# Kernel tuning notes

Measured on AMD Instinct MI355X. Metric: run time of the kernel, lower is better.

The kernel has to match this reference:

```python
import jax, jax.numpy as jnp
import numpy as np

B, C, D = 16384, 1000, 512
CLAMP_MIN = 1e-12
CLAMP_MAX = 1e12


def setup_inputs() -> dict:
    key = jax.random.key(0)
    k1, k2, k3 = jax.random.split(key, 3)
    x = jax.random.normal(k1, (B, D), dtype=jnp.float32)
    labels = jax.random.randint(k2, (B,), 0, C, dtype=jnp.int64)
    # centers param: n_classes != feat_dim -> normal init (as in _init_centers)
    centers = jax.random.normal(k3, (C, D), dtype=jnp.float32)
    return {"x": x, "labels": labels, "centers": centers}


def reference(x, labels, centers):
    batch_size = x.shape[0]
    n_classes = centers.shape[0]
    x_sq = jnp.sum(x * x, axis=1, keepdims=True)            # [B, 1]
    c_sq = jnp.sum(centers * centers, axis=1)[None, :]      # [1, C]
    distmat = x_sq + c_sq - 2.0 * (x @ centers.T)           # [B, C]
    # one-hot mask on true label
    mask = (labels[:, None] == jnp.arange(n_classes)[None, :]).astype(distmat.dtype)
    # NOTE: torch code clamps AFTER masking, so masked-out zeros become 1e-12
    # and each contributes 1e-12 to the sum -- reproduce that faithfully.
    dist = jnp.clip(distmat * mask, CLAMP_MIN, CLAMP_MAX)
    loss = jnp.sum(dist) / batch_size
    return loss
```

## Files before the change

### kernel.cpp

```cpp
#include <hip/hip_runtime.h>


#define B_ROWS    16384
#define C_CLASSES 1000
#define D_DIM     512
#define S1_BLOCKS 1024

__global__ __launch_bounds__(256) void center_loss_stage1(
    const float* __restrict__ x,
    const int*   __restrict__ labels,
    const float* __restrict__ centers,
    float*       __restrict__ partials)
{
    const int tid   = threadIdx.x;
    const int wave  = tid >> 6;
    const int lane  = tid & 63;
    const int gwave = blockIdx.x * 4 + wave;
    const int nwaves = gridDim.x * 4;

    float waveAcc = 0.0f;

    for (int row = gwave; row < B_ROWS; row += nwaves) {
        const int lab = labels[row];
        const float4* __restrict__ xr =
            (const float4*)(x + (size_t)row * D_DIM);
        const float4* __restrict__ cr =
            (const float4*)(centers + (size_t)lab * D_DIM);

        float4 xa = xr[lane];
        float4 xb = xr[lane + 64];
        float4 ca = cr[lane];
        float4 cb = cr[lane + 64];

        float d0 = xa.x - ca.x, d1 = xa.y - ca.y;
        float d2 = xa.z - ca.z, d3 = xa.w - ca.w;
        float e0 = xb.x - cb.x, e1 = xb.y - cb.y;
        float e2 = xb.z - cb.z, e3 = xb.w - cb.w;

        float s = d0*d0 + d1*d1 + d2*d2 + d3*d3
                + e0*e0 + e1*e1 + e2*e2 + e3*e3;

        #pragma unroll
        for (int off = 32; off > 0; off >>= 1)
            s += __shfl_down(s, off, 64);

        if (lane == 0) {
            s = fminf(fmaxf(s, 1e-12f), 1e12f);
            waveAcc += s;
        }
    }

    __shared__ float lds[4];
    if (lane == 0) lds[wave] = waveAcc;
    __syncthreads();
    if (tid == 0)
        partials[blockIdx.x] = lds[0] + lds[1] + lds[2] + lds[3];
}

__global__ __launch_bounds__(256) void center_loss_stage2(
    const float* __restrict__ partials,
    float*       __restrict__ out)
{
    const int tid  = threadIdx.x;
    const int wave = tid >> 6;
    const int lane = tid & 63;

    float s = 0.0f;
    for (int i = tid; i < S1_BLOCKS; i += 256)
        s += partials[i];

    #pragma unroll
    for (int off = 32; off > 0; off >>= 1)
        s += __shfl_down(s, off, 64);

    __shared__ float lds[4];
    if (lane == 0) lds[wave] = s;
    __syncthreads();
    if (tid == 0) {
        float tot = lds[0] + lds[1] + lds[2] + lds[3];
        tot += (float)B_ROWS * (float)(C_CLASSES - 1) * 1e-12f;
        out[0] = tot / (float)B_ROWS;
    }
}

extern "C" void kernel_launch(void* const* d_in, const int* in_sizes, int n_in,
                              void* d_out, int out_size, void* d_ws, size_t ws_size,
                              hipStream_t stream) {
    const float* x       = (const float*)d_in[0];
    const int*   labels  = (const int*)d_in[1];
    const float* centers = (const float*)d_in[2];
    float*       out     = (float*)d_out;
    float*       partials = (float*)d_ws;

    center_loss_stage1<<<S1_BLOCKS, 256, 0, stream>>>(x, labels, centers, partials);
    center_loss_stage2<<<1, 256, 0, stream>>>(partials, out);
}
```

Before: 79.92 us.

## Fuse two-stage reduction into single kernel with last-block atomic finalize

Merges the per-block partial kernel and the final reduction kernel into one launch. The last block to finish, detected with an atomic counter, sums all partials. Each wave now processes exactly two rows with all loads issued up front, instead of a grid-stride loop, which raises memory-level parallelism. The grid doubles to 2048 blocks. In exchange, a memset is needed to reset the counter, and the change depends on correct acquire/release ordering between blocks.

```diff
diff --git a/kernel.cpp b/kernel.cpp
--- a/kernel.cpp
+++ b/kernel.cpp
@@ -4,82 +4,91 @@
 #define B_ROWS    16384
 #define C_CLASSES 1000
 #define D_DIM     512
-#define S1_BLOCKS 1024
+#define GRID      2048
 
-__global__ __launch_bounds__(256) void center_loss_stage1(
+__global__ __launch_bounds__(256) void center_loss_fused(
     const float* __restrict__ x,
     const int*   __restrict__ labels,
     const float* __restrict__ centers,
-    float*       __restrict__ partials)
-{
-    const int tid   = threadIdx.x;
-    const int wave  = tid >> 6;
-    const int lane  = tid & 63;
-    const int gwave = blockIdx.x * 4 + wave;
-    const int nwaves = gridDim.x * 4;
-
-    float waveAcc = 0.0f;
-
-    for (int row = gwave; row < B_ROWS; row += nwaves) {
-        const int lab = labels[row];
-        const float4* __restrict__ xr =
-            (const float4*)(x + (size_t)row * D_DIM);
-        const float4* __restrict__ cr =
-            (const float4*)(centers + (size_t)lab * D_DIM);
-
-        float4 xa = xr[lane];
-        float4 xb = xr[lane + 64];
-        float4 ca = cr[lane];
-        float4 cb = cr[lane + 64];
-
-        float d0 = xa.x - ca.x, d1 = xa.y - ca.y;
-        float d2 = xa.z - ca.z, d3 = xa.w - ca.w;
-        float e0 = xb.x - cb.x, e1 = xb.y - cb.y;
-        float e2 = xb.z - cb.z, e3 = xb.w - cb.w;
-
-        float s = d0*d0 + d1*d1 + d2*d2 + d3*d3
-                + e0*e0 + e1*e1 + e2*e2 + e3*e3;
-
-        #pragma unroll
-        for (int off = 32; off > 0; off >>= 1)
-            s += __shfl_down(s, off, 64);
-
-        if (lane == 0) {
-            s = fminf(fmaxf(s, 1e-12f), 1e12f);
-            waveAcc += s;
-        }
-    }
-
-    __shared__ float lds[4];
-    if (lane == 0) lds[wave] = waveAcc;
-    __syncthreads();
-    if (tid == 0)
-        partials[blockIdx.x] = lds[0] + lds[1] + lds[2] + lds[3];
-}
-
-__global__ __launch_bounds__(256) void center_loss_stage2(
-    const float* __restrict__ partials,
-    float*       __restrict__ out)
+    float*       __restrict__ out,
+    float*       __restrict__ partials,
+    unsigned int* __restrict__ counter)
 {
     const int tid  = threadIdx.x;
     const int wave = tid >> 6;
     const int lane = tid & 63;
+    const int row0 = (blockIdx.x * 4 + wave) * 2;
 
-    float s = 0.0f;
-    for (int i = tid; i < S1_BLOCKS; i += 256)
-        s += partials[i];
+    const int lab0 = labels[row0];
+    const int lab1 = labels[row0 + 1];
+
+    const float4* __restrict__ xr0 = (const float4*)(x + (size_t)row0 * D_DIM);
+    const float4* __restrict__ xr1 = (const float4*)(x + (size_t)(row0 + 1) * D_DIM);
+    const float4* __restrict__ cr0 = (const float4*)(centers + (size_t)lab0 * D_DIM);
+    const float4* __restrict__ cr1 = (const float4*)(centers + (size_t)lab1 * D_DIM);
+
+    float4 xa0 = xr0[lane];
+    float4 xb0 = xr0[lane + 64];
+    float4 xa1 = xr1[lane];
+    float4 xb1 = xr1[lane + 64];
+    float4 ca0 = cr0[lane];
+    float4 cb0 = cr0[lane + 64];
+    float4 ca1 = cr1[lane];
+    float4 cb1 = cr1[lane + 64];
+
+    float acc;
+    {
+        float d0 = xa0.x - ca0.x, d1 = xa0.y - ca0.y;
+        float d2 = xa0.z - ca0.z, d3 = xa0.w - ca0.w;
+        float e0 = xb0.x - cb0.x, e1 = xb0.y - cb0.y;
+        float e2 = xb0.z - cb0.z, e3 = xb0.w - cb0.w;
+        acc = d0*d0 + d1*d1 + d2*d2 + d3*d3
+            + e0*e0 + e1*e1 + e2*e2 + e3*e3;
+    }
+    {
+        float d0 = xa1.x - ca1.x, d1 = xa1.y - ca1.y;
+        float d2 = xa1.z - ca1.z, d3 = xa1.w - ca1.w;
+        float e0 = xb1.x - cb1.x, e1 = xb1.y - cb1.y;
+        float e2 = xb1.z - cb1.z, e3 = xb1.w - cb1.w;
+        acc += d0*d0 + d1*d1 + d2*d2 + d3*d3
+             + e0*e0 + e1*e1 + e2*e2 + e3*e3;
+    }
 
     #pragma unroll
     for (int off = 32; off > 0; off >>= 1)
-        s += __shfl_down(s, off, 64);
+        acc += __shfl_down(acc, off, 64);
 
-    __shared__ float lds[4];
-    if (lane == 0) lds[wave] = s;
+    __shared__ float wsum[4];
+    if (lane == 0) wsum[wave] = acc;
     __syncthreads();
+
+    __shared__ bool isLast;
     if (tid == 0) {
-        float tot = lds[0] + lds[1] + lds[2] + lds[3];
-        tot += (float)B_ROWS * (float)(C_CLASSES - 1) * 1e-12f;
-        out[0] = tot / (float)B_ROWS;
+        float blockSum = wsum[0] + wsum[1] + wsum[2] + wsum[3];
+        __hip_atomic_store(&partials[blockIdx.x], blockSum,
+                           __ATOMIC_RELAXED, __HIP_MEMORY_SCOPE_AGENT);
+        unsigned prev = __hip_atomic_fetch_add(counter, 1u,
+                           __ATOMIC_ACQ_REL, __HIP_MEMORY_SCOPE_AGENT);
+        isLast = (prev == GRID - 1);
+    }
+    __syncthreads();
+
+    if (isLast) {
+        float v = 0.0f;
+        #pragma unroll
+        for (int i = 0; i < GRID / 256; ++i)
+            v += __hip_atomic_load(&partials[tid + i * 256],
+                                   __ATOMIC_RELAXED, __HIP_MEMORY_SCOPE_AGENT);
+        #pragma unroll
+        for (int off = 32; off > 0; off >>= 1)
+            v += __shfl_down(v, off, 64);
+        if (lane == 0) wsum[wave] = v;
+        __syncthreads();
+        if (tid == 0) {
+            float tot = wsum[0] + wsum[1] + wsum[2] + wsum[3];
+            tot += (float)B_ROWS * (float)(C_CLASSES - 1) * 1e-12f;
+            out[0] = tot / (float)B_ROWS;
+        }
     }
 }
 
@@ -90,8 +99,12 @@
     const int*   labels  = (const int*)d_in[1];
     const float* centers = (const float*)d_in[2];
     float*       out     = (float*)d_out;
-    float*       partials = (float*)d_ws;
 
-    center_loss_stage1<<<S1_BLOCKS, 256, 0, stream>>>(x, labels, centers, partials);
-    center_loss_stage2<<<1, 256, 0, stream>>>(partials, out);
+    unsigned int* counter  = (unsigned int*)d_ws;
+    float*        partials = (float*)((char*)d_ws + 256);
+
+    hipMemsetAsync(d_ws, 0, 4, stream);
+
+    center_loss_fused<<<GRID, 256, 0, stream>>>(x, labels, centers, out,
+                                                partials, counter);
 }
```

Result: slower. 137.9 us (+72.6%).
